# Kernel optimization log

Hardware: AMD Instinct MI355X
Metric: run time of the kernel (lower is better)

Reference implementation:

```python
import jax, jax.numpy as jnp
import numpy as np

EMB = 1024
HEADS = 16
HEAD_DIM = EMB // HEADS
B, S = 4, 2048


def setup_inputs() -> dict:
    key = jax.random.key(0)
    ks = jax.random.split(key, 9)
    sc = 1.0 / np.sqrt(EMB)
    x = jax.random.normal(ks[0], (B, S, EMB), dtype=jnp.float32)
    Wq = jax.random.normal(ks[1], (EMB, EMB), dtype=jnp.float32) * sc
    bq = jax.random.normal(ks[2], (EMB,), dtype=jnp.float32) * 0.02
    Wk = jax.random.normal(ks[3], (EMB, EMB), dtype=jnp.float32) * sc
    bk = jax.random.normal(ks[4], (EMB,), dtype=jnp.float32) * 0.02
    Wv = jax.random.normal(ks[5], (EMB, EMB), dtype=jnp.float32) * sc
    bv = jax.random.normal(ks[6], (EMB,), dtype=jnp.float32) * 0.02
    Wo = jax.random.normal(ks[7], (EMB, EMB), dtype=jnp.float32) * sc
    bo = jax.random.normal(ks[8], (EMB,), dtype=jnp.float32) * 0.02
    # causal mask: 1 where allowed (lower triangular), 0 elsewhere
    causal_mask = jnp.tril(jnp.ones((S, S), dtype=jnp.int32))[None, None]
    return {"x": x, "Wq": Wq, "bq": bq, "Wk": Wk, "bk": bk,
            "Wv": Wv, "bv": bv, "Wo": Wo, "bo": bo,
            "causal_mask": causal_mask}


def reference(x, Wq, bq, Wk, bk, Wv, bv, Wo, bo, causal_mask):
    bs, seq, _ = x.shape
    # nn.Linear: x @ W.T + b; then view [bs, seq, H, hd] and transpose to [bs, H, seq, hd]
    def proj(W, b):
        return (x @ W.T + b).reshape(bs, seq, HEADS, HEAD_DIM).transpose(0, 2, 1, 3)
    q, k, v = proj(Wq, bq), proj(Wk, bk), proj(Wv, bv)
    scale = 1.0 / np.sqrt(HEAD_DIM).astype(np.float32)
    dots = jnp.einsum('bhqd,bhkd->bhqk', q, k) * scale  # [B, H, S, S]
    dots = jnp.where(causal_mask == 0, -jnp.inf, dots)
    attn = jax.nn.softmax(dots, axis=-1)
    out = jnp.einsum('bhqk,bhkd->bhqd', attn, v)  # [B, H, S, hd]
    out = out.transpose(0, 2, 1, 3).reshape(bs, seq, EMB)
    return out @ Wo.T + bo
```

## Files before the change

### kernel.cpp

```cpp
#include <hip/hip_runtime.h>
#include <hip/hip_bf16.h>

typedef __attribute__((ext_vector_type(8))) short short8;
typedef __attribute__((ext_vector_type(4))) float floatx4;

#define B_    4
#define S_    2048
#define EMB_  1024
#define NH_   16
#define HD_   64

#if __has_builtin(__builtin_amdgcn_exp2f)
#define EXP2F(x) __builtin_amdgcn_exp2f(x)
#else
#define EXP2F(x) exp2f(x)
#endif

__device__ __forceinline__ void async_cp16(const void* g, void* l) {
  __builtin_amdgcn_global_load_lds(
      (const __attribute__((address_space(1))) unsigned int*)g,
      (__attribute__((address_space(3))) unsigned int*)l, 16, 0, 0);
}

__device__ __forceinline__ ushort4 cvt4(const float4 f) {
  __bf16 t[4] = {(__bf16)f.x, (__bf16)f.y, (__bf16)f.z, (__bf16)f.w};
  return *(const ushort4*)t;
}

__global__ __launch_bounds__(256)
void cvt_kernel(const float* __restrict__ x,
                const float* __restrict__ wq, const float* __restrict__ wk,
                const float* __restrict__ wv, const float* __restrict__ wo,
                const float* __restrict__ bq, const float* __restrict__ bk,
                const float* __restrict__ bv,
                __bf16* __restrict__ xb, __bf16* __restrict__ Wcat,
                __bf16* __restrict__ Wob, float* __restrict__ bcat)
{
  const int NX4 = 2097152;
  const int NW4 = 262144;
  int g = blockIdx.x * 256 + threadIdx.x;
  if (g < NX4) {
    *(ushort4*)(xb + (size_t)g * 4) = cvt4(*(const float4*)(x + (size_t)g * 4));
    return;
  }
  g -= NX4;
  if (g < 3 * NW4) {
    const float* src = (g < NW4) ? wq : (g < 2 * NW4) ? wk : wv;
    const int gg = (g < NW4) ? g : (g < 2 * NW4) ? g - NW4 : g - 2 * NW4;
    *(ushort4*)(Wcat + (size_t)g * 4) = cvt4(*(const float4*)(src + (size_t)gg * 4));
    return;
  }
  g -= 3 * NW4;
  if (g < NW4) {
    *(ushort4*)(Wob + (size_t)g * 4) = cvt4(*(const float4*)(wo + (size_t)g * 4));
    return;
  }
  g -= NW4;
  if (g < 768) {
    const float* src = (g < 256) ? bq : (g < 512) ? bk : bv;
    *(float4*)(bcat + (size_t)g * 4) = *(const float4*)(src + (size_t)(g & 255) * 4);
  }
}

__global__ __launch_bounds__(256)
void gemm_qkv_kernel(const __bf16* __restrict__ A, const __bf16* __restrict__ W,
                     const float* __restrict__ bcat,
                     __bf16* __restrict__ Qb, __bf16* __restrict__ Kb,
                     __bf16* __restrict__ Vb)
{
  __shared__ __attribute__((aligned(16))) __bf16 As[128 * 32];
  __shared__ __attribute__((aligned(16))) __bf16 Ws[128 * 32];
  const int tid  = threadIdx.x;
  const int wave = tid >> 6, lane = tid & 63;
  const int l15  = lane & 15, quad = lane >> 4;
  const int wm   = wave >> 1, wn = wave & 1;
  const int bm   = blockIdx.y * 128;
  const int bn   = blockIdx.x * 128;
  const int widx = bn >> 10;
  const float QS = 0.180336880f;

  floatx4 acc[4][4];
#pragma unroll
  for (int i = 0; i < 4; ++i)
#pragma unroll
    for (int j = 0; j < 4; ++j) acc[i][j] = (floatx4){0.f, 0.f, 0.f, 0.f};

  const int srow = tid >> 2;
  const int scol = (tid & 3) << 3;
  const __bf16* Ag = A + (size_t)(bm + srow) * 1024 + scol;
  const __bf16* Wg = W + (size_t)(bn + srow) * 1024 + scol;
  __bf16* AsD = As + tid * 8;
  __bf16* WsD = Ws + tid * 8;

  for (int k0 = 0; k0 < 1024; k0 += 32) {
    __syncthreads();
    async_cp16(Ag + k0,             AsD);
    async_cp16(Ag + k0 + 64 * 1024, AsD + 2048);
    async_cp16(Wg + k0,             WsD);
    async_cp16(Wg + k0 + 64 * 1024, WsD + 2048);
    __syncthreads();
    short8 af[4], wf[4];
#pragma unroll
    for (int mi = 0; mi < 4; ++mi)
      af[mi] = *(const short8*)(As + ((wm * 64 + mi * 16 + l15) << 5) + (quad << 3));
#pragma unroll
    for (int ni = 0; ni < 4; ++ni)
      wf[ni] = *(const short8*)(Ws + ((wn * 64 + ni * 16 + l15) << 5) + (quad << 3));
#pragma unroll
    for (int mi = 0; mi < 4; ++mi)
#pragma unroll
      for (int ni = 0; ni < 4; ++ni)
        acc[mi][ni] = __builtin_amdgcn_mfma_f32_16x16x32_bf16(af[mi], wf[ni], acc[mi][ni], 0, 0, 0);
  }

#pragma unroll
  for (int ni = 0; ni < 4; ++ni) {
    const int n  = bn + wn * 64 + ni * 16 + l15;
    const float bvb = bcat[n];
    const int np = n & 1023;
    const int h = np >> 6, d = np & 63;
#pragma unroll
    for (int mi = 0; mi < 4; ++mi) {
      const int m0 = bm + wm * 64 + mi * 16 + quad * 4;
      const int b = m0 >> 11, s0 = m0 & 2047;
      floatx4 v = acc[mi][ni];
      if (widx == 0) {
        const size_t base = (size_t)(b * 16 + h) * (S_ * 64) + d;
#pragma unroll
        for (int r = 0; r < 4; ++r)
          Qb[base + (size_t)(s0 + r) * 64] = (__bf16)((v[r] + bvb) * QS);
      } else if (widx == 1) {
        const size_t base = (size_t)(b * 16 + h) * (S_ * 64) + d;
#pragma unroll
        for (int r = 0; r < 4; ++r)
          Kb[base + (size_t)(s0 + r) * 64] = (__bf16)(v[r] + bvb);
      } else {
        const size_t base = ((size_t)(b * 16 + h) * 64 + d) * S_ + s0;
        union { ushort4 u4; unsigned short u[4]; } pk;
#pragma unroll
        for (int r = 0; r < 4; ++r) {
          __bf16 hv = (__bf16)(v[r] + bvb);
          pk.u[r] = *(unsigned short*)&hv;
        }
        *(ushort4*)(Vb + base) = pk.u4;
      }
    }
  }
}

__global__ __launch_bounds__(256, 4)
void attn_kernel(__bf16* __restrict__ Q, const __bf16* __restrict__ K,
                 const __bf16* __restrict__ Vt)
{
  __shared__ __attribute__((aligned(16))) __bf16 Ks[64 * 72];
  __shared__ __attribute__((aligned(16))) __bf16 Vs[80 * 72];
  __shared__ __attribute__((aligned(16))) __bf16 Ps[4][16 * 72];

  const int tid  = threadIdx.x;
  const int wave = tid >> 6, lane = tid & 63;
  const int l15  = lane & 15, quad = lane >> 4;
  const int qtA  = blockIdx.x, bh = blockIdx.y;
  const size_t hb = (size_t)bh * (S_ * 64);
  const float MASKV = -1.0e30f;

  for (int idx = tid; idx < 16 * 72; idx += 256)
    Vs[64 * 72 + idx] = (idx < 72) ? (__bf16)1.0f : (__bf16)0.0f;

  for (int qsel = 0; qsel < 2; ++qsel) {
    const int qt = qsel ? (31 - qtA) : qtA;
    const int q0 = qt * 64;
    const int qw = q0 + wave * 16;

    short8 aq[2];
#pragma unroll
    for (int kk = 0; kk < 2; ++kk)
      aq[kk] = *(const short8*)(Q + hb + (size_t)(qw + l15) * 64 + kk * 32 + quad * 8);

    floatx4 oacc[4];
#pragma unroll
    for (int j = 0; j < 4; ++j) oacc[j] = (floatx4){0.f, 0.f, 0.f, 0.f};
    floatx4 lacc = (floatx4){0.f, 0.f, 0.f, 0.f};
    float mst[4];
#pragma unroll
    for (int r = 0; r < 4; ++r) mst[r] = MASKV;

    for (int kt = 0; kt <= qt; ++kt) {
      __syncthreads();
      {
        const int r = tid >> 3;
        const int c = (tid & 7) << 3;
#pragma unroll
        for (int p = 0; p < 2; ++p) {
          const int row = r + p * 32;
          *(uint4*)(&Ks[row * 72 + c]) = *(const uint4*)(K  + hb + (size_t)(kt * 64 + row) * 64 + c);
          *(uint4*)(&Vs[row * 72 + c]) = *(const uint4*)(Vt + hb + (size_t)row * S_ + kt * 64 + c);
        }
      }
      __syncthreads();

      floatx4 sacc[4];
#pragma unroll
      for (int j = 0; j < 4; ++j) sacc[j] = (floatx4){0.f, 0.f, 0.f, 0.f};
#pragma unroll
      for (int kk = 0; kk < 2; ++kk) {
        short8 bk[4];
#pragma unroll
        for (int ni = 0; ni < 4; ++ni)
          bk[ni] = *(const short8*)(&Ks[(ni * 16 + l15) * 72 + kk * 32 + quad * 8]);
#pragma unroll
        for (int ni = 0; ni < 4; ++ni)
          sacc[ni] = __builtin_amdgcn_mfma_f32_16x16x32_bf16(aq[kk], bk[ni], sacc[ni], 0, 0, 0);
      }

      const bool needmask = (kt == qt);
      const int sc0 = kt * 64 + l15;
#pragma unroll
      for (int r = 0; r < 4; ++r) {
        const int qg = qw + quad * 4 + r;
        float z[4];
        if (needmask) {
#pragma unroll
          for (int ni = 0; ni < 4; ++ni) {
            float zz = sacc[ni][r];
            if (sc0 + ni * 16 > qg) zz = MASKV;
            z[ni] = zz;
          }
        } else {
#pragma unroll
          for (int ni = 0; ni < 4; ++ni) z[ni] = sacc[ni][r];
        }
        float tmax = fmaxf(fmaxf(z[0], z[1]), fmaxf(z[2], z[3]));
        tmax = fmaxf(tmax, __shfl_xor(tmax, 1));
        tmax = fmaxf(tmax, __shfl_xor(tmax, 2));
        tmax = fmaxf(tmax, __shfl_xor(tmax, 4));
        tmax = fmaxf(tmax, __shfl_xor(tmax, 8));
        const float mold = mst[r];
        const float mnew = fmaxf(mold, tmax);
        mst[r] = mnew;
        const float alpha = EXP2F(mold - mnew);
#pragma unroll
        for (int ni = 0; ni < 4; ++ni) {
          const float p = EXP2F(z[ni] - mnew);
          Ps[wave][(quad * 4 + r) * 72 + ni * 16 + l15] = (__bf16)p;
        }
#pragma unroll
        for (int ni = 0; ni < 4; ++ni) oacc[ni][r] *= alpha;
        lacc[r] *= alpha;
      }

      __syncthreads();

#pragma unroll
      for (int kk = 0; kk < 2; ++kk) {
        const short8 ap = *(const short8*)(&Ps[wave][l15 * 72 + kk * 32 + quad * 8]);
        short8 bv[4];
#pragma unroll
        for (int ni = 0; ni < 4; ++ni)
          bv[ni] = *(const short8*)(&Vs[(ni * 16 + l15) * 72 + kk * 32 + quad * 8]);
        const short8 bl = *(const short8*)(&Vs[(64 + l15) * 72 + kk * 32 + quad * 8]);
#pragma unroll
        for (int ni = 0; ni < 4; ++ni)
          oacc[ni] = __builtin_amdgcn_mfma_f32_16x16x32_bf16(ap, bv[ni], oacc[ni], 0, 0, 0);
        lacc = __builtin_amdgcn_mfma_f32_16x16x32_bf16(ap, bl, lacc, 0, 0, 0);
      }
    }

#pragma unroll
    for (int r = 0; r < 4; ++r) {
      const float lv  = __shfl(lacc[r], lane & 48);
      const float inv = 1.0f / fmaxf(lv, 1e-20f);
      const int qg = qw + quad * 4 + r;
      const size_t rowb = hb + (size_t)qg * 64;
#pragma unroll
      for (int ni = 0; ni < 4; ++ni)
        Q[rowb + ni * 16 + l15] = (__bf16)(oacc[ni][r] * inv);
    }
  }
}

__global__ __launch_bounds__(256)
void gemm_o_kernel(const __bf16* __restrict__ A, const __bf16* __restrict__ W,
                   const float* __restrict__ bias, float* __restrict__ out)
{
  __shared__ __attribute__((aligned(16))) __bf16 As[128 * 32];
  __shared__ __attribute__((aligned(16))) __bf16 Ws[128 * 32];
  const int tid  = threadIdx.x;
  const int wave = tid >> 6, lane = tid & 63;
  const int l15  = lane & 15, quad = lane >> 4;
  const int wm   = wave >> 1, wn = wave & 1;
  const int bm   = blockIdx.y * 128;
  const int bn   = blockIdx.x * 128;

  floatx4 acc[4][4];
#pragma unroll
  for (int i = 0; i < 4; ++i)
#pragma unroll
    for (int j = 0; j < 4; ++j) acc[i][j] = (floatx4){0.f, 0.f, 0.f, 0.f};

  const int srow = tid >> 2;
  const int scol = (tid & 3) << 3;
  const __bf16* Wg = W + (size_t)(bn + srow) * 1024 + scol;
  const int bb = bm >> 11;
  const int ss = (bm & 2047) + srow;
  __bf16* AsD = As + tid * 8;
  __bf16* WsD = Ws + tid * 8;

  for (int k0 = 0; k0 < 1024; k0 += 32) {
    const int c = k0 + scol, h = c >> 6, dd = c & 63;
    const __bf16* pa0 = A + (((size_t)(bb * 16 + h) * S_) + ss) * 64 + dd;
    __syncthreads();
    async_cp16(pa0,           AsD);
    async_cp16(pa0 + 64 * 64, AsD + 2048);
    async_cp16(Wg + k0,             WsD);
    async_cp16(Wg + k0 + 64 * 1024, WsD + 2048);
    __syncthreads();

    short8 af[4], wf[4];
#pragma unroll
    for (int mi = 0; mi < 4; ++mi)
      af[mi] = *(const short8*)(As + ((wm * 64 + mi * 16 + l15) << 5) + (quad << 3));
#pragma unroll
    for (int ni = 0; ni < 4; ++ni)
      wf[ni] = *(const short8*)(Ws + ((wn * 64 + ni * 16 + l15) << 5) + (quad << 3));
#pragma unroll
    for (int mi = 0; mi < 4; ++mi)
#pragma unroll
      for (int ni = 0; ni < 4; ++ni)
        acc[mi][ni] = __builtin_amdgcn_mfma_f32_16x16x32_bf16(af[mi], wf[ni], acc[mi][ni], 0, 0, 0);
  }

#pragma unroll
  for (int ni = 0; ni < 4; ++ni) {
    const int n = bn + wn * 64 + ni * 16 + l15;
    const float bvb = bias[n];
#pragma unroll
    for (int mi = 0; mi < 4; ++mi) {
      const int m0 = bm + wm * 64 + mi * 16 + quad * 4;
      floatx4 v = acc[mi][ni];
#pragma unroll
      for (int r = 0; r < 4; ++r)
        out[(size_t)(m0 + r) * 1024 + n] = v[r] + bvb;
    }
  }
}

extern "C" void kernel_launch(void* const* d_in, const int* in_sizes, int n_in,
                              void* d_out, int out_size, void* d_ws, size_t ws_size,
                              hipStream_t stream) {
  const float* x  = (const float*)d_in[0];
  const float* Wq = (const float*)d_in[1];
  const float* bq = (const float*)d_in[2];
  const float* Wk = (const float*)d_in[3];
  const float* bk = (const float*)d_in[4];
  const float* Wv = (const float*)d_in[5];
  const float* bv = (const float*)d_in[6];
  const float* Wo = (const float*)d_in[7];
  const float* bo = (const float*)d_in[8];

  const size_t BUF = (size_t)B_ * NH_ * S_ * HD_;
  __bf16* ws   = (__bf16*)d_ws;
  __bf16* xb   = ws;
  __bf16* Wcat = ws + 8388608;
  __bf16* Wob  = ws + 11534336;
  __bf16* Qb   = ws + 12582912;
  float*  bcat = (float*)(ws + 20971520);
  __bf16* Kb   = (__bf16*)d_out;
  __bf16* Vb   = (__bf16*)d_out + BUF;

  dim3 blk(256);
  cvt_kernel<<<12291, blk, 0, stream>>>(x, Wq, Wk, Wv, Wo, bq, bk, bv,
                                        xb, Wcat, Wob, bcat);
  gemm_qkv_kernel<<<dim3(24, 64), blk, 0, stream>>>(xb, Wcat, bcat, Qb, Kb, Vb);
  attn_kernel<<<dim3(16, 64), blk, 0, stream>>>(Qb, Kb, Vb);
  gemm_o_kernel<<<dim3(8, 64), blk, 0, stream>>>(Qb, Wob, bo, (float*)d_out);
}
```

Before: 308.3 us.

## Process paired causal query tiles together sharing K/V loads with register prefetch

After: 547.4 us. +77.6%, slower.

```diff
diff --git a/kernel.cpp b/kernel.cpp
--- a/kernel.cpp
+++ b/kernel.cpp
@@ -10,11 +10,7 @@
 #define NH_   16
 #define HD_   64
 
-#if __has_builtin(__builtin_amdgcn_exp2f)
-#define EXP2F(x) __builtin_amdgcn_exp2f(x)
-#else
 #define EXP2F(x) exp2f(x)
-#endif
 
 __device__ __forceinline__ void async_cp16(const void* g, void* l) {
   __builtin_amdgcn_global_load_lds(
@@ -159,121 +155,140 @@
   const int tid  = threadIdx.x;
   const int wave = tid >> 6, lane = tid & 63;
   const int l15  = lane & 15, quad = lane >> 4;
-  const int qtA  = blockIdx.x, bh = blockIdx.y;
+  const int bh   = blockIdx.x;
+  const int qtL  = blockIdx.y;
+  const int qtH  = 31 - qtL;
   const size_t hb = (size_t)bh * (S_ * 64);
   const float MASKV = -1.0e30f;
 
   for (int idx = tid; idx < 16 * 72; idx += 256)
     Vs[64 * 72 + idx] = (idx < 72) ? (__bf16)1.0f : (__bf16)0.0f;
 
-  for (int qsel = 0; qsel < 2; ++qsel) {
-    const int qt = qsel ? (31 - qtA) : qtA;
-    const int q0 = qt * 64;
-    const int qw = q0 + wave * 16;
-
-    short8 aq[2];
-#pragma unroll
-    for (int kk = 0; kk < 2; ++kk)
-      aq[kk] = *(const short8*)(Q + hb + (size_t)(qw + l15) * 64 + kk * 32 + quad * 8);
-
-    floatx4 oacc[4];
-#pragma unroll
-    for (int j = 0; j < 4; ++j) oacc[j] = (floatx4){0.f, 0.f, 0.f, 0.f};
-    floatx4 lacc = (floatx4){0.f, 0.f, 0.f, 0.f};
-    float mst[4];
-#pragma unroll
-    for (int r = 0; r < 4; ++r) mst[r] = MASKV;
-
-    for (int kt = 0; kt <= qt; ++kt) {
-      __syncthreads();
-      {
-        const int r = tid >> 3;
-        const int c = (tid & 7) << 3;
-#pragma unroll
-        for (int p = 0; p < 2; ++p) {
-          const int row = r + p * 32;
-          *(uint4*)(&Ks[row * 72 + c]) = *(const uint4*)(K  + hb + (size_t)(kt * 64 + row) * 64 + c);
-          *(uint4*)(&Vs[row * 72 + c]) = *(const uint4*)(Vt + hb + (size_t)row * S_ + kt * 64 + c);
-        }
+  const int qwL = qtL * 64 + wave * 16;
+  const int qwH = qtH * 64 + wave * 16;
+  short8 aqL[2], aqH[2];
+#pragma unroll
+  for (int kk = 0; kk < 2; ++kk) {
+    aqL[kk] = *(const short8*)(Q + hb + (size_t)(qwL + l15) * 64 + kk * 32 + quad * 8);
+    aqH[kk] = *(const short8*)(Q + hb + (size_t)(qwH + l15) * 64 + kk * 32 + quad * 8);
+  }
+
+  floatx4 oaccL[4], oaccH[4];
+#pragma unroll
+  for (int j = 0; j < 4; ++j) {
+    oaccL[j] = (floatx4){0.f, 0.f, 0.f, 0.f};
+    oaccH[j] = (floatx4){0.f, 0.f, 0.f, 0.f};
+  }
+  floatx4 laccL = (floatx4){0.f, 0.f, 0.f, 0.f};
+  floatx4 laccH = (floatx4){0.f, 0.f, 0.f, 0.f};
+  float mstL[4], mstH[4];
+#pragma unroll
+  for (int r = 0; r < 4; ++r) { mstL[r] = MASKV; mstH[r] = MASKV; }
+
+  const int sr = tid >> 3;
+  const int sc = (tid & 7) << 3;
+  uint4 kreg[2], vreg[2];
+#pragma unroll
+  for (int p = 0; p < 2; ++p) {
+    const int row = sr + p * 32;
+    kreg[p] = *(const uint4*)(K  + hb + (size_t)(0 * 64 + row) * 64 + sc);
+    vreg[p] = *(const uint4*)(Vt + hb + (size_t)row * S_ + 0 * 64 + sc);
+  }
+
+  auto tile = [&](const short8* aq, floatx4* oacc, floatx4& lacc, float* mst,
+                  const int qw, const int kt, const bool domask) {
+    floatx4 sacc[4];
+#pragma unroll
+    for (int j = 0; j < 4; ++j) sacc[j] = (floatx4){0.f, 0.f, 0.f, 0.f};
+#pragma unroll
+    for (int kk = 0; kk < 2; ++kk) {
+      short8 bk[4];
+#pragma unroll
+      for (int ni = 0; ni < 4; ++ni)
+        bk[ni] = *(const short8*)(&Ks[(ni * 16 + l15) * 72 + kk * 32 + quad * 8]);
+#pragma unroll
+      for (int ni = 0; ni < 4; ++ni)
+        sacc[ni] = __builtin_amdgcn_mfma_f32_16x16x32_bf16(aq[kk], bk[ni], sacc[ni], 0, 0, 0);
+    }
+    const int sc0 = kt * 64 + l15;
+#pragma unroll
+    for (int r = 0; r < 4; ++r) {
+      const int qg = qw + quad * 4 + r;
+      float z[4];
+#pragma unroll
+      for (int ni = 0; ni < 4; ++ni) {
+        float zz = sacc[ni][r];
+        if (domask && (sc0 + ni * 16 > qg)) zz = MASKV;
+        z[ni] = zz;
       }
-      __syncthreads();
-
-      floatx4 sacc[4];
-#pragma unroll
-      for (int j = 0; j < 4; ++j) sacc[j] = (floatx4){0.f, 0.f, 0.f, 0.f};
-#pragma unroll
-      for (int kk = 0; kk < 2; ++kk) {
-        short8 bk[4];
-#pragma unroll
-        for (int ni = 0; ni < 4; ++ni)
-          bk[ni] = *(const short8*)(&Ks[(ni * 16 + l15) * 72 + kk * 32 + quad * 8]);
-#pragma unroll
-        for (int ni = 0; ni < 4; ++ni)
-          sacc[ni] = __builtin_amdgcn_mfma_f32_16x16x32_bf16(aq[kk], bk[ni], sacc[ni], 0, 0, 0);
+      float tmax = fmaxf(fmaxf(z[0], z[1]), fmaxf(z[2], z[3]));
+      tmax = fmaxf(tmax, __shfl_xor(tmax, 1));
+      tmax = fmaxf(tmax, __shfl_xor(tmax, 2));
+      tmax = fmaxf(tmax, __shfl_xor(tmax, 4));
+      tmax = fmaxf(tmax, __shfl_xor(tmax, 8));
+      const float mold = mst[r];
+      const float mnew = fmaxf(mold, tmax);
+      mst[r] = mnew;
+      const float alpha = EXP2F(mold - mnew);
+#pragma unroll
+      for (int ni = 0; ni < 4; ++ni) {
+        const float p = EXP2F(z[ni] - mnew);
+        Ps[wave][(quad * 4 + r) * 72 + ni * 16 + l15] = (__bf16)p;
       }
-
-      const bool needmask = (kt == qt);
-      const int sc0 = kt * 64 + l15;
-#pragma unroll
-      for (int r = 0; r < 4; ++r) {
-        const int qg = qw + quad * 4 + r;
-        float z[4];
-        if (needmask) {
-#pragma unroll
-          for (int ni = 0; ni < 4; ++ni) {
-            float zz = sacc[ni][r];
-            if (sc0 + ni * 16 > qg) zz = MASKV;
-            z[ni] = zz;
-          }
-        } else {
-#pragma unroll
-          for (int ni = 0; ni < 4; ++ni) z[ni] = sacc[ni][r];
-        }
-        float tmax = fmaxf(fmaxf(z[0], z[1]), fmaxf(z[2], z[3]));
-        tmax = fmaxf(tmax, __shfl_xor(tmax, 1));
-        tmax = fmaxf(tmax, __shfl_xor(tmax, 2));
-        tmax = fmaxf(tmax, __shfl_xor(tmax, 4));
-        tmax = fmaxf(tmax, __shfl_xor(tmax, 8));
-        const float mold = mst[r];
-        const float mnew = fmaxf(mold, tmax);
-        mst[r] = mnew;
-        const float alpha = EXP2F(mold - mnew);
-#pragma unroll
-        for (int ni = 0; ni < 4; ++ni) {
-          const float p = EXP2F(z[ni] - mnew);
-          Ps[wave][(quad * 4 + r) * 72 + ni * 16 + l15] = (__bf16)p;
-        }
-#pragma unroll
-        for (int ni = 0; ni < 4; ++ni) oacc[ni][r] *= alpha;
-        lacc[r] *= alpha;
+#pragma unroll
+      for (int ni = 0; ni < 4; ++ni) oacc[ni][r] *= alpha;
+      lacc[r] *= alpha;
+    }
+#pragma unroll
+    for (int kk = 0; kk < 2; ++kk) {
+      const short8 ap = *(const short8*)(&Ps[wave][l15 * 72 + kk * 32 + quad * 8]);
+      short8 bv[4];
+#pragma unroll
+      for (int ni = 0; ni < 4; ++ni)
+        bv[ni] = *(const short8*)(&Vs[(ni * 16 + l15) * 72 + kk * 32 + quad * 8]);
+      const short8 bl = *(const short8*)(&Vs[(64 + l15) * 72 + kk * 32 + quad * 8]);
+#pragma unroll
+      for (int ni = 0; ni < 4; ++ni)
+        oacc[ni] = __builtin_amdgcn_mfma_f32_16x16x32_bf16(ap, bv[ni], oacc[ni], 0, 0, 0);
+      lacc = __builtin_amdgcn_mfma_f32_16x16x32_bf16(ap, bl, lacc, 0, 0, 0);
+    }
+  };
+
+  for (int kt = 0; kt <= qtH; ++kt) {
+    __syncthreads();
+#pragma unroll
+    for (int p = 0; p < 2; ++p) {
+      const int row = sr + p * 32;
+      *(uint4*)(&Ks[row * 72 + sc]) = kreg[p];
+      *(uint4*)(&Vs[row * 72 + sc]) = vreg[p];
+    }
+    __syncthreads();
+    if (kt < qtH) {
+      const int kn = kt + 1;
+#pragma unroll
+      for (int p = 0; p < 2; ++p) {
+        const int row = sr + p * 32;
+        kreg[p] = *(const uint4*)(K  + hb + (size_t)(kn * 64 + row) * 64 + sc);
+        vreg[p] = *(const uint4*)(Vt + hb + (size_t)row * S_ + kn * 64 + sc);
       }
-
-      __syncthreads();
-
-#pragma unroll
-      for (int kk = 0; kk < 2; ++kk) {
-        const short8 ap = *(const short8*)(&Ps[wave][l15 * 72 + kk * 32 + quad * 8]);
-        short8 bv[4];
-#pragma unroll
-        for (int ni = 0; ni < 4; ++ni)
-          bv[ni] = *(const short8*)(&Vs[(ni * 16 + l15) * 72 + kk * 32 + quad * 8]);
-        const short8 bl = *(const short8*)(&Vs[(64 + l15) * 72 + kk * 32 + quad * 8]);
-#pragma unroll
-        for (int ni = 0; ni < 4; ++ni)
-          oacc[ni] = __builtin_amdgcn_mfma_f32_16x16x32_bf16(ap, bv[ni], oacc[ni], 0, 0, 0);
-        lacc = __builtin_amdgcn_mfma_f32_16x16x32_bf16(ap, bl, lacc, 0, 0, 0);
-      }
-    }
-
-#pragma unroll
-    for (int r = 0; r < 4; ++r) {
-      const float lv  = __shfl(lacc[r], lane & 48);
-      const float inv = 1.0f / fmaxf(lv, 1e-20f);
-      const int qg = qw + quad * 4 + r;
-      const size_t rowb = hb + (size_t)qg * 64;
-#pragma unroll
-      for (int ni = 0; ni < 4; ++ni)
-        Q[rowb + ni * 16 + l15] = (__bf16)(oacc[ni][r] * inv);
+    }
+    tile(aqH, oaccH, laccH, mstH, qwH, kt, kt == qtH);
+    if (kt <= qtL)
+      tile(aqL, oaccL, laccL, mstL, qwL, kt, kt == qtL);
+  }
+
+#pragma unroll
+  for (int r = 0; r < 4; ++r) {
+    const float lvH = __shfl(laccH[r], lane & 48);
+    const float lvL = __shfl(laccL[r], lane & 48);
+    const float invH = 1.0f / fmaxf(lvH, 1e-20f);
+    const float invL = 1.0f / fmaxf(lvL, 1e-20f);
+    const size_t rowH = hb + (size_t)(qwH + quad * 4 + r) * 64;
+    const size_t rowL = hb + (size_t)(qwL + quad * 4 + r) * 64;
+#pragma unroll
+    for (int ni = 0; ni < 4; ++ni) {
+      Q[rowH + ni * 16 + l15] = (__bf16)(oaccH[ni][r] * invH);
+      Q[rowL + ni * 16 + l15] = (__bf16)(oaccL[ni][r] * invL);
     }
   }
 }
@@ -371,6 +386,6 @@
   cvt_kernel<<<12291, blk, 0, stream>>>(x, Wq, Wk, Wv, Wo, bq, bk, bv,
                                         xb, Wcat, Wob, bcat);
   gemm_qkv_kernel<<<dim3(24, 64), blk, 0, stream>>>(xb, Wcat, bcat, Qb, Kb, Vb);
-  attn_kernel<<<dim3(16, 64), blk, 0, stream>>>(Qb, Kb, Vb);
+  attn_kernel<<<dim3(64, 16), blk, 0, stream>>>(Qb, Kb, Vb);
   gemm_o_kernel<<<dim3(8, 64), blk, 0, stream>>>(Qb, Wob, bo, (float*)d_out);
 }
```

## Prefetch next K/V tile into registers and drop a barrier in attention

Applied to the files above, without the earlier changes.

Result: slower. 372.4 us (+20.8%).

```diff
diff --git a/kernel.cpp b/kernel.cpp
--- a/kernel.cpp
+++ b/kernel.cpp
@@ -10,11 +10,7 @@
 #define NH_   16
 #define HD_   64
 
-#if __has_builtin(__builtin_amdgcn_exp2f)
-#define EXP2F(x) __builtin_amdgcn_exp2f(x)
-#else
 #define EXP2F(x) exp2f(x)
-#endif
 
 __device__ __forceinline__ void async_cp16(const void* g, void* l) {
   __builtin_amdgcn_global_load_lds(
@@ -159,12 +155,16 @@
   const int tid  = threadIdx.x;
   const int wave = tid >> 6, lane = tid & 63;
   const int l15  = lane & 15, quad = lane >> 4;
-  const int qtA  = blockIdx.x, bh = blockIdx.y;
+  const int bh   = blockIdx.x;
+  const int qtA  = blockIdx.y;
   const size_t hb = (size_t)bh * (S_ * 64);
   const float MASKV = -1.0e30f;
 
   for (int idx = tid; idx < 16 * 72; idx += 256)
     Vs[64 * 72 + idx] = (idx < 72) ? (__bf16)1.0f : (__bf16)0.0f;
+
+  const int sr = tid >> 3;
+  const int sc = (tid & 7) << 3;
 
   for (int qsel = 0; qsel < 2; ++qsel) {
     const int qt = qsel ? (31 - qtA) : qtA;
@@ -184,19 +184,32 @@
 #pragma unroll
     for (int r = 0; r < 4; ++r) mst[r] = MASKV;
 
+    uint4 kreg[2], vreg[2];
+#pragma unroll
+    for (int p = 0; p < 2; ++p) {
+      const int row = sr + p * 32;
+      kreg[p] = *(const uint4*)(K  + hb + (size_t)row * 64 + sc);
+      vreg[p] = *(const uint4*)(Vt + hb + (size_t)row * S_ + sc);
+    }
+
     for (int kt = 0; kt <= qt; ++kt) {
       __syncthreads();
-      {
-        const int r = tid >> 3;
-        const int c = (tid & 7) << 3;
+#pragma unroll
+      for (int p = 0; p < 2; ++p) {
+        const int row = sr + p * 32;
+        *(uint4*)(&Ks[row * 72 + sc]) = kreg[p];
+        *(uint4*)(&Vs[row * 72 + sc]) = vreg[p];
+      }
+      __syncthreads();
+      if (kt < qt) {
+        const int kn = kt + 1;
 #pragma unroll
         for (int p = 0; p < 2; ++p) {
-          const int row = r + p * 32;
-          *(uint4*)(&Ks[row * 72 + c]) = *(const uint4*)(K  + hb + (size_t)(kt * 64 + row) * 64 + c);
-          *(uint4*)(&Vs[row * 72 + c]) = *(const uint4*)(Vt + hb + (size_t)row * S_ + kt * 64 + c);
+          const int row = sr + p * 32;
+          kreg[p] = *(const uint4*)(K  + hb + (size_t)(kn * 64 + row) * 64 + sc);
+          vreg[p] = *(const uint4*)(Vt + hb + (size_t)row * S_ + kn * 64 + sc);
         }
       }
-      __syncthreads();
 
       floatx4 sacc[4];
 #pragma unroll
@@ -247,8 +260,6 @@
         for (int ni = 0; ni < 4; ++ni) oacc[ni][r] *= alpha;
         lacc[r] *= alpha;
       }
-
-      __syncthreads();
 
 #pragma unroll
       for (int kk = 0; kk < 2; ++kk) {
@@ -371,6 +382,6 @@
   cvt_kernel<<<12291, blk, 0, stream>>>(x, Wq, Wk, Wv, Wo, bq, bk, bv,
                                         xb, Wcat, Wob, bcat);
   gemm_qkv_kernel<<<dim3(24, 64), blk, 0, stream>>>(xb, Wcat, bcat, Qb, Kb, Vb);
-  attn_kernel<<<dim3(16, 64), blk, 0, stream>>>(Qb, Kb, Vb);
+  attn_kernel<<<dim3(64, 16), blk, 0, stream>>>(Qb, Kb, Vb);
   gemm_o_kernel<<<dim3(8, 64), blk, 0, stream>>>(Qb, Wob, bo, (float*)d_out);
 }
```

## Stage attention K/V tiles with async LDS loads and swizzled layout

Applied to the files above, without the earlier changes.

Result: no change. 310.6 us (+0.8%).

```diff
diff --git a/kernel.cpp b/kernel.cpp
--- a/kernel.cpp
+++ b/kernel.cpp
@@ -10,11 +10,7 @@
 #define NH_   16
 #define HD_   64
 
-#if __has_builtin(__builtin_amdgcn_exp2f)
-#define EXP2F(x) __builtin_amdgcn_exp2f(x)
-#else
 #define EXP2F(x) exp2f(x)
-#endif
 
 __device__ __forceinline__ void async_cp16(const void* g, void* l) {
   __builtin_amdgcn_global_load_lds(
@@ -152,24 +148,29 @@
 void attn_kernel(__bf16* __restrict__ Q, const __bf16* __restrict__ K,
                  const __bf16* __restrict__ Vt)
 {
-  __shared__ __attribute__((aligned(16))) __bf16 Ks[64 * 72];
-  __shared__ __attribute__((aligned(16))) __bf16 Vs[80 * 72];
+  __shared__ __attribute__((aligned(16))) __bf16 Ks[64 * 64];
+  __shared__ __attribute__((aligned(16))) __bf16 Vs[64 * 64];
   __shared__ __attribute__((aligned(16))) __bf16 Ps[4][16 * 72];
 
   const int tid  = threadIdx.x;
   const int wave = tid >> 6, lane = tid & 63;
   const int l15  = lane & 15, quad = lane >> 4;
-  const int qtA  = blockIdx.x, bh = blockIdx.y;
+  const int bh   = blockIdx.x;
+  const int qtA  = blockIdx.y;
   const size_t hb = (size_t)bh * (S_ * 64);
   const float MASKV = -1.0e30f;
 
-  for (int idx = tid; idx < 16 * 72; idx += 256)
-    Vs[64 * 72 + idx] = (idx < 72) ? (__bf16)1.0f : (__bf16)0.0f;
+  const short ONE = (short)0x3F80;
+  const short8 ones8 = {ONE, ONE, ONE, ONE, ONE, ONE, ONE, ONE};
+
+  const int rho  = lane >> 3;
+  const int cswz = ((lane & 7) ^ rho) * 8;
+  const int fsw0 = ((quad    ) ^ (l15 & 7)) * 8;
+  const int fsw1 = ((quad + 4) ^ (l15 & 7)) * 8;
 
   for (int qsel = 0; qsel < 2; ++qsel) {
     const int qt = qsel ? (31 - qtA) : qtA;
-    const int q0 = qt * 64;
-    const int qw = q0 + wave * 16;
+    const int qw = qt * 64 + wave * 16;
 
     short8 aq[2];
 #pragma unroll
@@ -186,15 +187,12 @@
 
     for (int kt = 0; kt <= qt; ++kt) {
       __syncthreads();
-      {
-        const int r = tid >> 3;
-        const int c = (tid & 7) << 3;
-#pragma unroll
-        for (int p = 0; p < 2; ++p) {
-          const int row = r + p * 32;
-          *(uint4*)(&Ks[row * 72 + c]) = *(const uint4*)(K  + hb + (size_t)(kt * 64 + row) * 64 + c);
-          *(uint4*)(&Vs[row * 72 + c]) = *(const uint4*)(Vt + hb + (size_t)row * S_ + kt * 64 + c);
-        }
+#pragma unroll
+      for (int t = 0; t < 2; ++t) {
+        const int rb = (t * 4 + wave) * 8 + rho;
+        const int ci = ((t * 4 + wave) * 64 + lane) * 8;
+        async_cp16(K  + hb + (size_t)(kt * 64 + rb) * 64 + cswz, &Ks[ci]);
+        async_cp16(Vt + hb + (size_t)rb * S_ + kt * 64 + cswz,   &Vs[ci]);
       }
       __syncthreads();
 
@@ -203,10 +201,11 @@
       for (int j = 0; j < 4; ++j) sacc[j] = (floatx4){0.f, 0.f, 0.f, 0.f};
 #pragma unroll
       for (int kk = 0; kk < 2; ++kk) {
+        const int fsw = kk ? fsw1 : fsw0;
         short8 bk[4];
 #pragma unroll
         for (int ni = 0; ni < 4; ++ni)
-          bk[ni] = *(const short8*)(&Ks[(ni * 16 + l15) * 72 + kk * 32 + quad * 8]);
+          bk[ni] = *(const short8*)(&Ks[(ni * 16 + l15) * 64 + fsw]);
 #pragma unroll
         for (int ni = 0; ni < 4; ++ni)
           sacc[ni] = __builtin_amdgcn_mfma_f32_16x16x32_bf16(aq[kk], bk[ni], sacc[ni], 0, 0, 0);
@@ -248,27 +247,24 @@
         lacc[r] *= alpha;
       }
 
-      __syncthreads();
-
 #pragma unroll
       for (int kk = 0; kk < 2; ++kk) {
+        const int fsw = kk ? fsw1 : fsw0;
         const short8 ap = *(const short8*)(&Ps[wave][l15 * 72 + kk * 32 + quad * 8]);
         short8 bv[4];
 #pragma unroll
         for (int ni = 0; ni < 4; ++ni)
-          bv[ni] = *(const short8*)(&Vs[(ni * 16 + l15) * 72 + kk * 32 + quad * 8]);
-        const short8 bl = *(const short8*)(&Vs[(64 + l15) * 72 + kk * 32 + quad * 8]);
+          bv[ni] = *(const short8*)(&Vs[(ni * 16 + l15) * 64 + fsw]);
 #pragma unroll
         for (int ni = 0; ni < 4; ++ni)
           oacc[ni] = __builtin_amdgcn_mfma_f32_16x16x32_bf16(ap, bv[ni], oacc[ni], 0, 0, 0);
-        lacc = __builtin_amdgcn_mfma_f32_16x16x32_bf16(ap, bl, lacc, 0, 0, 0);
+        lacc = __builtin_amdgcn_mfma_f32_16x16x32_bf16(ap, ones8, lacc, 0, 0, 0);
       }
     }
 
 #pragma unroll
     for (int r = 0; r < 4; ++r) {
-      const float lv  = __shfl(lacc[r], lane & 48);
-      const float inv = 1.0f / fmaxf(lv, 1e-20f);
+      const float inv = 1.0f / fmaxf(lacc[r], 1e-20f);
       const int qg = qw + quad * 4 + r;
       const size_t rowb = hb + (size_t)qg * 64;
 #pragma unroll
@@ -371,6 +367,6 @@
   cvt_kernel<<<12291, blk, 0, stream>>>(x, Wq, Wk, Wv, Wo, bq, bk, bv,
                                         xb, Wcat, Wob, bcat);
   gemm_qkv_kernel<<<dim3(24, 64), blk, 0, stream>>>(xb, Wcat, bcat, Qb, Kb, Vb);
-  attn_kernel<<<dim3(16, 64), blk, 0, stream>>>(Qb, Kb, Vb);
+  attn_kernel<<<dim3(64, 16), blk, 0, stream>>>(Qb, Kb, Vb);
   gemm_o_kernel<<<dim3(8, 64), blk, 0, stream>>>(Qb, Wob, bo, (float*)d_out);
 }
```
